# Performance work log

Measured on AMD Instinct MI355X. Metric: run time of the kernel, lower is better.

The kernel has to match this reference:

```python
import jax, jax.numpy as jnp
import numpy as np

NUM_NODES = 200000
B = 65536          # n_id batch size
E = 131072         # events per direction
D_MEM = 128
D_RAW = 128
D_TIME = 128
T_MAX = 1000000


def setup_inputs() -> dict:
    key = jax.random.key(0)
    ks = jax.random.split(key, 16)
    inp = {
        'memory': jax.random.normal(ks[0], (NUM_NODES, D_MEM), jnp.float32),
        'last_update': jax.random.randint(ks[1], (NUM_NODES,), 0, 1000, jnp.int64),
        'n_id': jnp.arange(B, dtype=jnp.int64),
        'src_s': jax.random.randint(ks[2], (E,), 0, B, jnp.int64),
        'dst_s': jax.random.randint(ks[3], (E,), 0, B, jnp.int64),
        't_s': jax.random.randint(ks[4], (E,), 0, T_MAX, jnp.int64),
        'raw_msg_s': jax.random.normal(ks[5], (E, D_RAW), jnp.float32),
        'src_d': jax.random.randint(ks[6], (E,), 0, B, jnp.int64),
        'dst_d': jax.random.randint(ks[7], (E,), 0, B, jnp.int64),
        't_d': jax.random.randint(ks[8], (E,), 0, T_MAX, jnp.int64),
        'raw_msg_d': jax.random.normal(ks[9], (E, D_RAW), jnp.float32),
        'w_time': jax.random.normal(ks[10], (D_TIME, 1), jnp.float32) * 0.1,
        'b_time': jax.random.normal(ks[11], (D_TIME,), jnp.float32) * 0.1,
        'W_ih': jax.random.normal(ks[12], (3 * D_MEM, 2 * D_MEM + D_RAW + D_TIME), jnp.float32) * 0.05,
        'W_hh': jax.random.normal(ks[13], (3 * D_MEM, D_MEM), jnp.float32) * 0.05,
        'b_ih': jax.random.normal(ks[14], (3 * D_MEM,), jnp.float32) * 0.05,
        'b_hh': jax.random.normal(ks[15], (3 * D_MEM,), jnp.float32) * 0.05,
    }
    return inp


def _time_enc(t_rel, w_time, b_time):
    # Linear(1, time_dim) followed by cos: cos(t * w + b)
    return jnp.cos(t_rel.astype(jnp.float32)[:, None] * w_time[:, 0][None, :] + b_time)


def reference(memory, last_update, n_id, src_s, dst_s, t_s, raw_msg_s,
              src_d, dst_d, t_d, raw_msg_d, w_time, b_time, W_ih, W_hh, b_ih, b_hh):
    nb = n_id.shape[0]
    # assoc: global node id -> local index within n_id
    assoc = jnp.zeros((memory.shape[0],), dtype=jnp.int32).at[n_id].set(
        jnp.arange(nb, dtype=jnp.int32))

    # source-side messages (IdentityMessage = concat)
    t_enc_s = _time_enc(t_s - last_update[src_s], w_time, b_time)
    msg_s = jnp.concatenate([memory[src_s], memory[dst_s], raw_msg_s, t_enc_s], axis=-1)

    # destination-side messages
    t_enc_d = _time_enc(t_d - last_update[dst_d], w_time, b_time)
    msg_d = jnp.concatenate([memory[dst_d], memory[src_d], raw_msg_d, t_enc_d], axis=-1)

    idx = jnp.concatenate([src_s, dst_d], axis=0)       # [2E] global ids
    msg = jnp.concatenate([msg_s, msg_d], axis=0)       # [2E, 512]
    t = jnp.concatenate([t_s, t_d], axis=0)             # [2E]
    loc = assoc[idx]                                     # [2E] local ids

    # LastAggregator: per local node, pick the message with max t (ties -> latest position)
    ne = t.shape[0]
    key = t * ne + jnp.arange(ne, dtype=t.dtype)         # encode (t, position)
    maxkey = jax.ops.segment_max(key, loc, num_segments=nb)
    count = jax.ops.segment_sum(jnp.ones_like(loc), loc, num_segments=nb)
    has = count > 0
    argm = jnp.where(has, maxkey % ne, 0)
    aggr = jnp.where(has[:, None], msg[argm], 0.0)       # [nb, 512]

    # GRUCell(x=aggr, h=memory[n_id])
    h = memory[n_id]
    gi = aggr @ W_ih.T + b_ih
    gh = h @ W_hh.T + b_hh
    gi_r, gi_z, gi_n = jnp.split(gi, 3, axis=-1)
    gh_r, gh_z, gh_n = jnp.split(gh, 3, axis=-1)
    r = jax.nn.sigmoid(gi_r + gh_r)
    z = jax.nn.sigmoid(gi_z + gh_z)
    n = jnp.tanh(gi_n + r * gh_n)
    new_memory = (1.0 - z) * n + z * h

    new_last_update = last_update.at[idx].set(t)[n_id]
    return new_memory, new_last_update
```

## Files before the change

### kernel.cpp

```cpp
#include <hip/hip_runtime.h>
#include <math.h>

#define NUM_NODES 200000
#define NB        65536
#define EV        131072
#define NE        (2*EV)
#define DM        128
#define KDIM      640
#define NO2       512
#define BM        128
#define BK        32
#define THREADS   1024

typedef float f32x4 __attribute__((ext_vector_type(4)));
typedef unsigned long long u64;

__device__ __forceinline__ float fcos_rev(float rev) {
    float r; asm("v_cos_f32 %0, %1" : "=v"(r) : "v"(rev)); return r;
}
__device__ __forceinline__ float fexp2(float x) {
    float r; asm("v_exp_f32 %0, %1" : "=v"(r) : "v"(x)); return r;
}
__device__ __forceinline__ float frcp(float x) {
    float r; asm("v_rcp_f32 %0, %1" : "=v"(r) : "v"(x)); return r;
}
__device__ __forceinline__ float fast_cos(float arg) {
    double rv = (double)arg * 0.15915494309189535;
    rv -= floor(rv);
    return fcos_rev((float)rv);
}
__device__ __forceinline__ float fsigmoid(float x) {
    x = fminf(fmaxf(x, -30.f), 30.f);
    float e = fexp2(-1.44269504088896f * x);
    return frcp(1.f + e);
}
__device__ __forceinline__ float ftanh_(float x) {
    x = fminf(fmaxf(x, -15.f), 15.f);
    float e = fexp2(-2.88539008177793f * x);
    return (1.f - e) * frcp(1.f + e);
}

#if defined(__has_builtin) && __has_builtin(__builtin_amdgcn_cvt_pk_fp8_f32)
__device__ __forceinline__ unsigned pack4_fp8(float f0, float f1, float f2, float f3) {
    int v = __builtin_amdgcn_cvt_pk_fp8_f32(f0, f1, 0, false);
    v = __builtin_amdgcn_cvt_pk_fp8_f32(f2, f3, v, true);
    return (unsigned)v;
}
#else
__device__ __forceinline__ unsigned enc1_fp8(float x) {
    unsigned u = __float_as_uint(x);
    unsigned s = (u >> 24) & 0x80u;
    float a = fabsf(x);
    if (!(a >= 0.001953125f)) return s;
    if (a > 448.f) a = 448.f;
    int e; float mf = frexpf(a, &e);
    int E = e + 6;
    int mant;
    if (E <= 0) {
        mant = (int)(a * 512.f + 0.5f);
        if (mant > 7) return s | 0x08u;
        return s | (unsigned)mant;
    }
    mant = (int)((mf * 2.f - 1.f) * 8.f + 0.5f);
    if (mant == 8) { mant = 0; ++E; }
    if (E > 15) { E = 15; mant = 6; }
    if (E == 15 && mant == 7) mant = 6;
    return s | (unsigned)(E << 3) | (unsigned)mant;
}
__device__ __forceinline__ unsigned pack4_fp8(float f0, float f1, float f2, float f3) {
    return enc1_fp8(f0) | (enc1_fp8(f1) << 8) | (enc1_fp8(f2) << 16) | (enc1_fp8(f3) << 24);
}
#endif

__global__ void event_scan_k(const int* __restrict__ src_s, const int* __restrict__ t_s,
                             const int* __restrict__ dst_d, const int* __restrict__ t_d,
                             u64* __restrict__ keyarr,
                             u64* __restrict__ lukey) {
    int e = blockIdx.x * 256 + threadIdx.x;
    if (e >= NE) return;
    int g, t;
    if (e < EV) { g = src_s[e];      t = t_s[e]; }
    else        { g = dst_d[e - EV]; t = t_d[e - EV]; }
    u64 key = ((u64)(unsigned)t << 18) + (u64)(unsigned)e + 1ull;
    atomicMax(&keyarr[g], key);
    u64 lk = ((u64)(unsigned)(e + 1) << 20) | (u64)(unsigned)t;
    atomicMax(&lukey[g], lk);
}

__global__ void build_w_k(const float* __restrict__ W_ih, const float* __restrict__ W_hh,
                          const float* __restrict__ b_ih, const float* __restrict__ b_hh,
                          unsigned char* __restrict__ wp8, float* __restrict__ bp) {
    int idx = blockIdx.x * 256 + threadIdx.x;
    if (idx >= NO2 * 80) return;
    int p = idx / 80, grp = idx - p * 80;
    int d = p >> 2, gate = p & 3;
    float f[8];
    #pragma unroll
    for (int j = 0; j < 8; ++j) {
        int c = grp * 8 + j;
        float v = 0.f;
        if (c < 512) {
            int row = (gate == 0) ? d : (gate == 1) ? 128 + d : (gate == 2) ? 256 + d : -1;
            if (row >= 0) v = W_ih[(size_t)row * 512 + c];
        } else {
            int ch = c - 512;
            int row = (gate == 0) ? d : (gate == 1) ? 128 + d : (gate == 3) ? 256 + d : -1;
            if (row >= 0) v = W_hh[(size_t)row * 128 + ch];
        }
        f[j] = v * 16.f;
    }
    unsigned lo = pack4_fp8(f[0], f[1], f[2], f[3]);
    unsigned hi = pack4_fp8(f[4], f[5], f[6], f[7]);
    u64 q = (u64)lo | ((u64)hi << 32);
    *(u64*)(wp8 + (size_t)(grp >> 2) * 16384 + (size_t)(grp & 3) * 4096 + (size_t)p * 8) = q;
    if (grp == 0) {
        float bv = (gate == 0) ? b_ih[d] + b_hh[d]
                 : (gate == 1) ? b_ih[128 + d] + b_hh[128 + d]
                 : (gate == 2) ? b_ih[256 + d] : b_hh[256 + d];
        bp[p] = bv;
    }
}

__global__ __launch_bounds__(THREADS, 4) void gemm_gru_k(
    const float* __restrict__ memory, const int* __restrict__ last_update,
    const int* __restrict__ src_s, const int* __restrict__ dst_s,
    const int* __restrict__ t_s, const float* __restrict__ raw_s,
    const int* __restrict__ src_d, const int* __restrict__ dst_d,
    const int* __restrict__ t_d, const float* __restrict__ raw_d,
    const float* __restrict__ w_time, const float* __restrict__ b_time,
    const unsigned char* __restrict__ wp8, const float* __restrict__ bp,
    const u64* __restrict__ keyarr, const u64* __restrict__ lukey,
    float* __restrict__ out_mem, float* __restrict__ out_lu)
{
    __shared__ __align__(16) char smem[132096];
    unsigned char* sA = (unsigned char*)smem;
    unsigned char* sB = (unsigned char*)(smem + 8192);
    float* sG = (float*)smem;
    float* sW = (float*)(smem + 40960);
    float* sBt= (float*)(smem + 41472);

    const int tid = threadIdx.x;
    const int m0  = blockIdx.x * BM;
    const int ln  = tid & 63, wid = tid >> 6;
    const int wm  = wid >> 3, wn = wid & 7;
    const int l2  = ln >> 4, rl = ln & 15;

    if (tid < DM) { sW[tid] = w_time[tid]; sBt[tid] = b_time[tid]; }

    const int ar = tid >> 3, ac = tid & 7;
    const int m  = m0 + ar;
    const u64 kk = keyarr[m];
    const int rv = (kk != 0ull);
    int a_ = 0, b_ = 0, t_ = 0;
    const float* pR = raw_s;
    if (kk) {
        int e = (int)((kk - 1ull) & (u64)(NE - 1));
        if (e < EV) { a_ = src_s[e]; b_ = dst_s[e]; t_ = t_s[e]; pR = raw_s + (size_t)e * DM; }
        else { int e2 = e - EV; a_ = dst_d[e2]; b_ = src_d[e2]; t_ = t_d[e2]; pR = raw_d + (size_t)e2 * DM; }
    }
    const float rt = rv ? (float)(t_ - last_update[a_]) : 0.f;
    const float* pA = memory + (size_t)a_ * DM;
    const float* pB = memory + (size_t)b_ * DM;
    const float* pH = memory + (size_t)m  * DM;

    float4 pv;
    auto PREF_A = [&](int step) {
        int s2 = step >> 2;
        if (s2 == 3) return;
        const float* base = (s2 == 0) ? pA : (s2 == 1) ? pB : (s2 == 2) ? pR : pH;
        pv = *(const float4*)(base + ((step & 3) << 5) + (ac << 2));
    };
    auto STAGE_B = [&](int step, int buf) {
        const unsigned char* src = wp8 + (size_t)step * 16384 + (size_t)tid * 16;
        __builtin_amdgcn_global_load_lds((const __attribute__((address_space(1))) void*)src,
            (__attribute__((address_space(3))) void*)(sB + buf * 16384 + tid * 16), 16, 0, 0);
    };
    auto WRITE_A = [&](int step, int buf) {
        int seg = step >> 2;
        float f0, f1, f2, f3;
        if (seg == 3) {
            int coff = ((step & 3) << 5) + (ac << 2);
            f0 = fast_cos(__fadd_rn(__fmul_rn(rt, sW[coff+0]), sBt[coff+0])) * 8.f;
            f1 = fast_cos(__fadd_rn(__fmul_rn(rt, sW[coff+1]), sBt[coff+1])) * 8.f;
            f2 = fast_cos(__fadd_rn(__fmul_rn(rt, sW[coff+2]), sBt[coff+2])) * 8.f;
            f3 = fast_cos(__fadd_rn(__fmul_rn(rt, sW[coff+3]), sBt[coff+3])) * 8.f;
        } else {
            f0 = pv.x * 8.f; f1 = pv.y * 8.f; f2 = pv.z * 8.f; f3 = pv.w * 8.f;
        }
        if (seg < 4 && !rv) { f0 = f1 = f2 = f3 = 0.f; }
        unsigned q = pack4_fp8(f0, f1, f2, f3);
        *(unsigned*)(sA + buf * 4096 + (ac >> 1) * 1024 + ar * 8 + (ac & 1) * 4) = q;
    };

    f32x4 acc[4][4];
    #pragma unroll
    for (int mf = 0; mf < 4; ++mf)
        #pragma unroll
        for (int nf = 0; nf < 4; ++nf)
            acc[mf][nf] = (f32x4){0.f, 0.f, 0.f, 0.f};

    PREF_A(0);
    WRITE_A(0, 0);
    STAGE_B(0, 0);
    PREF_A(1);
    asm volatile("s_waitcnt vmcnt(1) lgkmcnt(0)" ::: "memory");
    __builtin_amdgcn_sched_barrier(0);
    __builtin_amdgcn_s_barrier();

    #pragma unroll
    for (int k = 0; k < 20; ++k) {
        const int cur = k & 1, nxt = cur ^ 1;

        long afr[4], bfr[4];
        #pragma unroll
        for (int mf = 0; mf < 4; ++mf)
            afr[mf] = *(const long*)(sA + cur * 4096 + l2 * 1024 + (wm * 64 + mf * 16 + rl) * 8);
        #pragma unroll
        for (int nf = 0; nf < 4; ++nf)
            bfr[nf] = *(const long*)(sB + cur * 16384 + l2 * 4096 + (wn * 64 + nf * 16 + rl) * 8);

        const bool pf = (k < 18) && (((k + 2) >> 2) != 3);
        if (k < 19) {
            WRITE_A(k + 1, nxt);
            __builtin_amdgcn_sched_barrier(0);
            STAGE_B(k + 1, nxt);
            __builtin_amdgcn_sched_barrier(0);
            if (pf) PREF_A(k + 2);
        }

        __builtin_amdgcn_s_setprio(1);
        #pragma unroll
        for (int mf = 0; mf < 4; ++mf)
            #pragma unroll
            for (int nf = 0; nf < 4; ++nf)
                acc[mf][nf] = __builtin_amdgcn_mfma_f32_16x16x32_fp8_fp8(
                    afr[mf], bfr[nf], acc[mf][nf], 0, 0, 0);
        __builtin_amdgcn_s_setprio(0);

        if (k < 19) {
            __builtin_amdgcn_sched_barrier(0);
            if (pf) asm volatile("s_waitcnt vmcnt(1) lgkmcnt(0)" ::: "memory");
            else    asm volatile("s_waitcnt vmcnt(0) lgkmcnt(0)" ::: "memory");
            __builtin_amdgcn_sched_barrier(0);
            __builtin_amdgcn_s_barrier();
        }
    }

    if (tid < BM) {
        u64 lk = lukey[m0 + tid];
        out_lu[m0 + tid] = lk ? (float)(unsigned)(lk & 0xFFFFFull)
                              : (float)last_update[m0 + tid];
    }
    __syncthreads();

    const float ds = 0.0078125f;
    #pragma unroll
    for (int p = 0; p < 2; ++p) {
        if (wm == p) {
            #pragma unroll
            for (int mf = 0; mf < 4; ++mf)
                #pragma unroll
                for (int nf = 0; nf < 4; ++nf)
                    #pragma unroll
                    for (int reg = 0; reg < 4; ++reg) {
                        int row = mf * 16 + l2 * 4 + reg;
                        int col = wn * 64 + nf * 16 + rl;
                        sG[row * 516 + col] = acc[mf][nf][reg] * ds;
                    }
        }
        __syncthreads();
        #pragma unroll
        for (int i = 0; i < 2; ++i) {
            int idx = tid + i * 1024;
            int row = idx >> 5, dq = idx & 31;
            int gm = m0 + p * 64 + row;
            const float* gr = sG + row * 516 + dq * 16;
            f32x4 g0 = *(const f32x4*)(gr + 0);
            f32x4 g1 = *(const f32x4*)(gr + 4);
            f32x4 g2 = *(const f32x4*)(gr + 8);
            f32x4 g3 = *(const f32x4*)(gr + 12);
            f32x4 bb0 = *(const f32x4*)(bp + dq * 16 + 0);
            f32x4 bb1 = *(const f32x4*)(bp + dq * 16 + 4);
            f32x4 bb2 = *(const f32x4*)(bp + dq * 16 + 8);
            f32x4 bb3 = *(const f32x4*)(bp + dq * 16 + 12);
            f32x4 h = *(const f32x4*)(memory + (size_t)gm * DM + dq * 4);
            f32x4 res;
            {
                float rg = fsigmoid(g0.x + bb0.x);
                float zg = fsigmoid(g0.y + bb0.y);
                float ng = ftanh_(g0.z + bb0.z + rg * (g0.w + bb0.w));
                res.x = (1.f - zg) * ng + zg * h.x;
            }
            {
                float rg = fsigmoid(g1.x + bb1.x);
                float zg = fsigmoid(g1.y + bb1.y);
                float ng = ftanh_(g1.z + bb1.z + rg * (g1.w + bb1.w));
                res.y = (1.f - zg) * ng + zg * h.y;
            }
            {
                float rg = fsigmoid(g2.x + bb2.x);
                float zg = fsigmoid(g2.y + bb2.y);
                float ng = ftanh_(g2.z + bb2.z + rg * (g2.w + bb2.w));
                res.z = (1.f - zg) * ng + zg * h.z;
            }
            {
                float rg = fsigmoid(g3.x + bb3.x);
                float zg = fsigmoid(g3.y + bb3.y);
                float ng = ftanh_(g3.z + bb3.z + rg * (g3.w + bb3.w));
                res.w = (1.f - zg) * ng + zg * h.w;
            }
            *(f32x4*)(out_mem + (size_t)gm * DM + dq * 4) = res;
        }
        if (p == 0) __syncthreads();
    }
}

extern "C" void kernel_launch(void* const* d_in, const int* in_sizes, int n_in,
                              void* d_out, int out_size, void* d_ws, size_t ws_size,
                              hipStream_t stream) {
    const float* memory      = (const float*)d_in[0];
    const int*   last_update = (const int*)d_in[1];
    const int*   src_s       = (const int*)d_in[3];
    const int*   dst_s       = (const int*)d_in[4];
    const int*   t_s         = (const int*)d_in[5];
    const float* raw_s       = (const float*)d_in[6];
    const int*   src_d       = (const int*)d_in[7];
    const int*   dst_d       = (const int*)d_in[8];
    const int*   t_d         = (const int*)d_in[9];
    const float* raw_d       = (const float*)d_in[10];
    const float* w_time      = (const float*)d_in[11];
    const float* b_time      = (const float*)d_in[12];
    const float* W_ih        = (const float*)d_in[13];
    const float* W_hh        = (const float*)d_in[14];
    const float* b_ih        = (const float*)d_in[15];
    const float* b_hh        = (const float*)d_in[16];

    char* ws = (char*)d_ws;
    u64* keyarr = (u64*)ws;
    u64* lukey  = (u64*)(ws + 524288);
    unsigned char* wp8 = (unsigned char*)(ws + 1048576);
    float* bp = (float*)(ws + 1376256);

    hipMemsetAsync(d_ws, 0, 1048576, stream);

    event_scan_k<<<NE / 256, 256, 0, stream>>>(src_s, t_s, dst_d, t_d, keyarr, lukey);
    build_w_k<<<(NO2 * 80 + 255) / 256, 256, 0, stream>>>(W_ih, W_hh, b_ih, b_hh, wp8, bp);

    float* out_mem = (float*)d_out;
    float* out_lu  = out_mem + (size_t)NB * DM;
    gemm_gru_k<<<NB / BM, THREADS, 0, stream>>>(memory, last_update,
        src_s, dst_s, t_s, raw_s, src_d, dst_d, t_d, raw_d,
        w_time, b_time, wp8, bp, keyarr, lukey, out_mem, out_lu);
}
```

Before: 87.79 us.

## Double the GEMM K-step and triple-buffer weight tiles in the fused GRU kernel

Raises the K tile of the fused FP8 gather-GEMM-GRU kernel from 32 to 64. The loop now runs 10 iterations, each doing two MFMA sub-steps, which halves the number of block-wide barriers. Weight tiles are triple-buffered in LDS and prefetched two steps ahead, with vmcnt waits retuned per iteration. Activation staging now uses wider 8-element gathers and packed 64-bit LDS writes. The activation pre-scale of 8 before FP8 quantization is dropped and the dequant factor is adjusted to match, which changes rounding behaviour. The B buffers take much more LDS, and the hand-tuned wait counts are fragile.

```diff
diff --git a/kernel.cpp b/kernel.cpp
--- a/kernel.cpp
+++ b/kernel.cpp
@@ -9,7 +9,7 @@
 #define KDIM      640
 #define NO2       512
 #define BM        128
-#define BK        32
+#define BK        64
 #define THREADS   1024
 
 typedef float f32x4 __attribute__((ext_vector_type(4)));
@@ -74,8 +74,7 @@
 
 __global__ void event_scan_k(const int* __restrict__ src_s, const int* __restrict__ t_s,
                              const int* __restrict__ dst_d, const int* __restrict__ t_d,
-                             u64* __restrict__ keyarr,
-                             u64* __restrict__ lukey) {
+                             u64* __restrict__ keyarr, u64* __restrict__ lukey) {
     int e = blockIdx.x * 256 + threadIdx.x;
     if (e >= NE) return;
     int g, t;
@@ -92,12 +91,12 @@
                           unsigned char* __restrict__ wp8, float* __restrict__ bp) {
     int idx = blockIdx.x * 256 + threadIdx.x;
     if (idx >= NO2 * 80) return;
-    int p = idx / 80, grp = idx - p * 80;
+    int p = idx / 80, g = idx - p * 80;
     int d = p >> 2, gate = p & 3;
     float f[8];
     #pragma unroll
     for (int j = 0; j < 8; ++j) {
-        int c = grp * 8 + j;
+        int c = g * 8 + j;
         float v = 0.f;
         if (c < 512) {
             int row = (gate == 0) ? d : (gate == 1) ? 128 + d : (gate == 2) ? 256 + d : -1;
@@ -112,8 +111,8 @@
     unsigned lo = pack4_fp8(f[0], f[1], f[2], f[3]);
     unsigned hi = pack4_fp8(f[4], f[5], f[6], f[7]);
     u64 q = (u64)lo | ((u64)hi << 32);
-    *(u64*)(wp8 + (size_t)(grp >> 2) * 16384 + (size_t)(grp & 3) * 4096 + (size_t)p * 8) = q;
-    if (grp == 0) {
+    *(u64*)(wp8 + (size_t)(g >> 3) * 32768 + (size_t)(g & 7) * 4096 + (size_t)p * 8) = q;
+    if (g == 0) {
         float bv = (gate == 0) ? b_ih[d] + b_hh[d]
                  : (gate == 1) ? b_ih[128 + d] + b_hh[128 + d]
                  : (gate == 2) ? b_ih[256 + d] : b_hh[256 + d];
@@ -134,10 +133,10 @@
 {
     __shared__ __align__(16) char smem[132096];
     unsigned char* sA = (unsigned char*)smem;
-    unsigned char* sB = (unsigned char*)(smem + 8192);
+    unsigned char* sB = (unsigned char*)(smem + 16384);
     float* sG = (float*)smem;
-    float* sW = (float*)(smem + 40960);
-    float* sBt= (float*)(smem + 41472);
+    float* sW = (float*)(smem + 114688);
+    float* sBt= (float*)(smem + 115200);
 
     const int tid = threadIdx.x;
     const int m0  = blockIdx.x * BM;
@@ -163,33 +162,45 @@
     const float* pB = memory + (size_t)b_ * DM;
     const float* pH = memory + (size_t)m  * DM;
 
-    float4 pv;
+    float4 pv0, pv1;
     auto PREF_A = [&](int step) {
-        int s2 = step >> 2;
-        if (s2 == 3) return;
-        const float* base = (s2 == 0) ? pA : (s2 == 1) ? pB : (s2 == 2) ? pR : pH;
-        pv = *(const float4*)(base + ((step & 3) << 5) + (ac << 2));
+        int seg = step >> 1;
+        if (seg == 3) return;
+        const float* base = (seg == 0) ? pA : (seg == 1) ? pB : (seg == 2) ? pR : pH;
+        int off = ((step & 1) << 6) + (ac << 3);
+        pv0 = *(const float4*)(base + off);
+        pv1 = *(const float4*)(base + off + 4);
     };
     auto STAGE_B = [&](int step, int buf) {
-        const unsigned char* src = wp8 + (size_t)step * 16384 + (size_t)tid * 16;
+        const unsigned char* src = wp8 + (size_t)step * 32768 + (size_t)tid * 16;
+        unsigned char* dst = sB + (size_t)buf * 32768 + (size_t)tid * 16;
         __builtin_amdgcn_global_load_lds((const __attribute__((address_space(1))) void*)src,
-            (__attribute__((address_space(3))) void*)(sB + buf * 16384 + tid * 16), 16, 0, 0);
+            (__attribute__((address_space(3))) void*)dst, 16, 0, 0);
+        __builtin_amdgcn_global_load_lds((const __attribute__((address_space(1))) void*)(src + 16384),
+            (__attribute__((address_space(3))) void*)(dst + 16384), 16, 0, 0);
     };
     auto WRITE_A = [&](int step, int buf) {
-        int seg = step >> 2;
-        float f0, f1, f2, f3;
+        int seg = step >> 1;
+        float f0, f1, f2, f3, f4, f5, f6, f7;
         if (seg == 3) {
-            int coff = ((step & 3) << 5) + (ac << 2);
-            f0 = fast_cos(__fadd_rn(__fmul_rn(rt, sW[coff+0]), sBt[coff+0])) * 8.f;
-            f1 = fast_cos(__fadd_rn(__fmul_rn(rt, sW[coff+1]), sBt[coff+1])) * 8.f;
-            f2 = fast_cos(__fadd_rn(__fmul_rn(rt, sW[coff+2]), sBt[coff+2])) * 8.f;
-            f3 = fast_cos(__fadd_rn(__fmul_rn(rt, sW[coff+3]), sBt[coff+3])) * 8.f;
+            int coff = ((step & 1) << 6) + (ac << 3);
+            f0 = fast_cos(__fadd_rn(__fmul_rn(rt, sW[coff+0]), sBt[coff+0]));
+            f1 = fast_cos(__fadd_rn(__fmul_rn(rt, sW[coff+1]), sBt[coff+1]));
+            f2 = fast_cos(__fadd_rn(__fmul_rn(rt, sW[coff+2]), sBt[coff+2]));
+            f3 = fast_cos(__fadd_rn(__fmul_rn(rt, sW[coff+3]), sBt[coff+3]));
+            f4 = fast_cos(__fadd_rn(__fmul_rn(rt, sW[coff+4]), sBt[coff+4]));
+            f5 = fast_cos(__fadd_rn(__fmul_rn(rt, sW[coff+5]), sBt[coff+5]));
+            f6 = fast_cos(__fadd_rn(__fmul_rn(rt, sW[coff+6]), sBt[coff+6]));
+            f7 = fast_cos(__fadd_rn(__fmul_rn(rt, sW[coff+7]), sBt[coff+7]));
         } else {
-            f0 = pv.x * 8.f; f1 = pv.y * 8.f; f2 = pv.z * 8.f; f3 = pv.w * 8.f;
-        }
-        if (seg < 4 && !rv) { f0 = f1 = f2 = f3 = 0.f; }
-        unsigned q = pack4_fp8(f0, f1, f2, f3);
-        *(unsigned*)(sA + buf * 4096 + (ac >> 1) * 1024 + ar * 8 + (ac & 1) * 4) = q;
+            f0 = pv0.x; f1 = pv0.y; f2 = pv0.z; f3 = pv0.w;
+            f4 = pv1.x; f5 = pv1.y; f6 = pv1.z; f7 = pv1.w;
+        }
+        if (seg < 4 && !rv) { f0=f1=f2=f3=f4=f5=f6=f7 = 0.f; }
+        unsigned lo = pack4_fp8(f0, f1, f2, f3);
+        unsigned hi = pack4_fp8(f4, f5, f6, f7);
+        u64 q = (u64)lo | ((u64)hi << 32);
+        *(u64*)(sA + buf * 8192 + ac * 1024 + ar * 8) = q;
     };
 
     f32x4 acc[4][4];
@@ -202,31 +213,35 @@
     PREF_A(0);
     WRITE_A(0, 0);
     STAGE_B(0, 0);
+    STAGE_B(1, 1);
     PREF_A(1);
-    asm volatile("s_waitcnt vmcnt(1) lgkmcnt(0)" ::: "memory");
+    asm volatile("s_waitcnt vmcnt(4) lgkmcnt(0)" ::: "memory");
     __builtin_amdgcn_sched_barrier(0);
     __builtin_amdgcn_s_barrier();
 
     #pragma unroll
-    for (int k = 0; k < 20; ++k) {
-        const int cur = k & 1, nxt = cur ^ 1;
-
-        long afr[4], bfr[4];
+    for (int k = 0; k < 10; ++k) {
+        const int av = k & 1, an = av ^ 1;
+        const int bv = k % 3;
+
+        const unsigned char* sAc = sA + av * 8192;
+        const unsigned char* sBc = sB + bv * 32768;
+
+        long afr0[4], bfr0[4];
         #pragma unroll
         for (int mf = 0; mf < 4; ++mf)
-            afr[mf] = *(const long*)(sA + cur * 4096 + l2 * 1024 + (wm * 64 + mf * 16 + rl) * 8);
+            afr0[mf] = *(const long*)(sAc + l2 * 1024 + (wm * 64 + mf * 16 + rl) * 8);
         #pragma unroll
         for (int nf = 0; nf < 4; ++nf)
-            bfr[nf] = *(const long*)(sB + cur * 16384 + l2 * 4096 + (wn * 64 + nf * 16 + rl) * 8);
-
-        const bool pf = (k < 18) && (((k + 2) >> 2) != 3);
-        if (k < 19) {
-            WRITE_A(k + 1, nxt);
-            __builtin_amdgcn_sched_barrier(0);
-            STAGE_B(k + 1, nxt);
-            __builtin_amdgcn_sched_barrier(0);
-            if (pf) PREF_A(k + 2);
-        }
+            bfr0[nf] = *(const long*)(sBc + l2 * 4096 + (wn * 64 + nf * 16 + rl) * 8);
+        __builtin_amdgcn_sched_barrier(0);
+
+        if (k < 9) WRITE_A(k + 1, an);
+        __builtin_amdgcn_sched_barrier(0);
+        if (k < 8) STAGE_B(k + 2, (k + 2) % 3);
+        __builtin_amdgcn_sched_barrier(0);
+        if (k < 8 && ((k + 2) >> 1) != 3) PREF_A(k + 2);
+        __builtin_amdgcn_sched_barrier(0);
 
         __builtin_amdgcn_s_setprio(1);
         #pragma unroll
@@ -234,13 +249,33 @@
             #pragma unroll
             for (int nf = 0; nf < 4; ++nf)
                 acc[mf][nf] = __builtin_amdgcn_mfma_f32_16x16x32_fp8_fp8(
-                    afr[mf], bfr[nf], acc[mf][nf], 0, 0, 0);
+                    afr0[mf], bfr0[nf], acc[mf][nf], 0, 0, 0);
         __builtin_amdgcn_s_setprio(0);
 
-        if (k < 19) {
+        long afr1[4], bfr1[4];
+        #pragma unroll
+        for (int mf = 0; mf < 4; ++mf)
+            afr1[mf] = *(const long*)(sAc + (4 + l2) * 1024 + (wm * 64 + mf * 16 + rl) * 8);
+        #pragma unroll
+        for (int nf = 0; nf < 4; ++nf)
+            bfr1[nf] = *(const long*)(sBc + (4 + l2) * 4096 + (wn * 64 + nf * 16 + rl) * 8);
+        __builtin_amdgcn_s_setprio(1);
+        #pragma unroll
+        for (int mf = 0; mf < 4; ++mf)
+            #pragma unroll
+            for (int nf = 0; nf < 4; ++nf)
+                acc[mf][nf] = __builtin_amdgcn_mfma_f32_16x16x32_fp8_fp8(
+                    afr1[mf], bfr1[nf], acc[mf][nf], 0, 0, 0);
+        __builtin_amdgcn_s_setprio(0);
+
+        if (k < 9) {
             __builtin_amdgcn_sched_barrier(0);
-            if (pf) asm volatile("s_waitcnt vmcnt(1) lgkmcnt(0)" ::: "memory");
-            else    asm volatile("s_waitcnt vmcnt(0) lgkmcnt(0)" ::: "memory");
+            if (k < 4 || k == 6 || k == 7)
+                asm volatile("s_waitcnt vmcnt(4) lgkmcnt(0)" ::: "memory");
+            else if (k == 4 || k == 5)
+                asm volatile("s_waitcnt vmcnt(2) lgkmcnt(0)" ::: "memory");
+            else
+                asm volatile("s_waitcnt vmcnt(0) lgkmcnt(0)" ::: "memory");
             __builtin_amdgcn_sched_barrier(0);
             __builtin_amdgcn_s_barrier();
         }
@@ -253,7 +288,7 @@
     }
     __syncthreads();
 
-    const float ds = 0.0078125f;
+    const float ds = 0.0625f;
     #pragma unroll
     for (int p = 0; p < 2; ++p) {
         if (wm == p) {
```

New measurement: 88.53 us. No clear change (+0.8%).
